# Optimization experiments

Hardware: AMD Instinct MI355X
Metric: run time of the kernel (lower is better)

## Reference

```python
import jax, jax.numpy as jnp
import numpy as np

B, D_IN, H, D_OUT = 8192, 1024, 4096, 1024


def setup_inputs() -> dict:
    key = jax.random.key(0)
    ks = jax.random.split(key, 8)
    return {
        "X": jax.random.normal(ks[0], (B, D_IN), jnp.float32),
        "state": jax.random.normal(ks[1], (B, H), jnp.float32),
        "W_in": jax.random.normal(ks[2], (H, D_IN), jnp.float32) * (2.0 / D_IN) ** 0.5,
        "b_in": jax.random.normal(ks[3], (H,), jnp.float32) * 0.1,
        "W_rec": jax.random.normal(ks[4], (H, H), jnp.float32) * (2.0 / H) ** 0.5,
        "b_rec": jax.random.normal(ks[5], (H,), jnp.float32) * 0.1,
        "W_out": jax.random.normal(ks[6], (D_OUT, H), jnp.float32) * (2.0 / H) ** 0.5,
        "b_out": jax.random.normal(ks[7], (D_OUT,), jnp.float32) * 0.1,
    }


def reference(X, state, W_in, b_in, W_rec, b_rec, W_out, b_out):
    # Single vanilla RNN cell step (ReLU recurrence), matching VanillaRNN.forward.
    # state: [B, H] = ReLU(X @ W_in^T + b_in + state @ W_rec^T + b_rec)
    new_state = jax.nn.relu(X @ W_in.T + b_in + state @ W_rec.T + b_rec)
    # out: [B, D_OUT] = ReLU(new_state @ W_out^T + b_out)
    out = jax.nn.relu(new_state @ W_out.T + b_out)
    return out, new_state
```

## Files before the change

### kernel.cpp

```cpp
#include <hip/hip_runtime.h>
#include <hip/hip_bf16.h>
#include <stdint.h>
#include <stddef.h>

#define BSZ  8192
#define DIN  1024
#define HH   4096
#define DOUT 1024

#define BM 128
#define BN 128
#define BK 32

typedef __attribute__((ext_vector_type(8))) short   frag8;
typedef __attribute__((ext_vector_type(4))) float   f32x4;
typedef __attribute__((ext_vector_type(8))) unsigned short u16x8;

__device__ __forceinline__ unsigned short f2bf_rne(float f) {
    union { float f; uint32_t u; } c; c.f = f;
    uint32_t u = c.u;
    return (unsigned short)((u + 0x7FFFu + ((u >> 16) & 1u)) >> 16);
}

__device__ __forceinline__ void cvt8(const float* __restrict__ s, unsigned short* __restrict__ d) {
    f32x4 v0 = *(const f32x4*)s;
    f32x4 v1 = *(const f32x4*)(s + 4);
    u16x8 o;
    o[0] = f2bf_rne(v0[0]); o[1] = f2bf_rne(v0[1]); o[2] = f2bf_rne(v0[2]); o[3] = f2bf_rne(v0[3]);
    o[4] = f2bf_rne(v1[0]); o[5] = f2bf_rne(v1[1]); o[6] = f2bf_rne(v1[2]); o[7] = f2bf_rne(v1[3]);
    *(u16x8*)d = o;
}

__global__ __launch_bounds__(256)
void cvt_f32_bf16(const float* __restrict__ src, unsigned short* __restrict__ dst, long n) {
    long i = ((long)blockIdx.x * 256 + threadIdx.x) * 8;
    if (i < n) cvt8(src + i, dst + i);
}

__global__ __launch_bounds__(256)
void cvt_all5(const float* __restrict__ s0, unsigned short* __restrict__ d0, long n0,
              const float* __restrict__ s1, unsigned short* __restrict__ d1, long n1,
              const float* __restrict__ s2, unsigned short* __restrict__ d2, long n2,
              const float* __restrict__ s3, unsigned short* __restrict__ d3, long n3,
              const float* __restrict__ s4, unsigned short* __restrict__ d4, long n4) {
    long i = ((long)blockIdx.x * 256 + threadIdx.x) * 8;
    if (i < n0) { cvt8(s0 + i, d0 + i); return; } i -= n0;
    if (i < n1) { cvt8(s1 + i, d1 + i); return; } i -= n1;
    if (i < n2) { cvt8(s2 + i, d2 + i); return; } i -= n2;
    if (i < n3) { cvt8(s3 + i, d3 + i); return; } i -= n3;
    if (i < n4) { cvt8(s4 + i, d4 + i); }
}

#define NX8  ((long)BSZ * DIN / 8)
#define NS8  ((long)BSZ * HH / 8)
#define NWI8 ((long)HH * DIN / 8)
#define NWR8 ((long)HH * HH / 8)
#define NWO8 ((long)DOUT * HH / 8)
#define NCVT_BLOCKS 32768

__global__ __launch_bounds__(256)
void cvt_pack(const float* __restrict__ X, const float* __restrict__ S,
              const float* __restrict__ Wi, const float* __restrict__ Wr,
              const float* __restrict__ Wo,
              unsigned short* __restrict__ XS, unsigned short* __restrict__ W1,
              unsigned short* __restrict__ Wob) {
    long i = (long)blockIdx.x * 256 + threadIdx.x;
    if (i < NX8)  { long r = i >> 7, c = i & 127; cvt8(X + i * 8, XS + r * 5120 + c * 8); return; }
    i -= NX8;
    if (i < NS8)  { long r = i >> 9, c = i & 511; cvt8(S + i * 8, XS + r * 5120 + 1024 + c * 8); return; }
    i -= NS8;
    if (i < NWI8) { long r = i >> 7, c = i & 127; cvt8(Wi + i * 8, W1 + r * 5120 + c * 8); return; }
    i -= NWI8;
    if (i < NWR8) { long r = i >> 9, c = i & 511; cvt8(Wr + i * 8, W1 + r * 5120 + 1024 + c * 8); return; }
    i -= NWR8;
    if (i < NWO8) { cvt8(Wo + i * 8, Wob + i * 8); }
}

__device__ __forceinline__ void glds16(const unsigned short* __restrict__ gp, short* lp) {
    __builtin_amdgcn_global_load_lds(
        (const __attribute__((address_space(1))) uint32_t*)gp,
        (__attribute__((address_space(3))) uint32_t*)lp, 16, 0, 0);
}

__device__ __forceinline__ void glds16v(const unsigned short* __restrict__ gp, void* lp) {
    __builtin_amdgcn_global_load_lds(
        (const __attribute__((address_space(1))) uint32_t*)gp,
        (__attribute__((address_space(3))) uint32_t*)lp, 16, 0, 0);
}

template<int C>
__device__ __forceinline__ void ktile_group(
    int kA, int kB,
    const unsigned short* __restrict__ gA, size_t a64,
    const unsigned short* __restrict__ gB, size_t b64,
    const char* Ar0, const char* Br0, char* ldsw,
    int aoff, int boff, f32x4 (&acc)[8][4])
{
    const char* Ar = Ar0 + C * 65536;
    const char* Br = Br0 + C * 65536;
    char* wA = ldsw + (C ^ 1) * 65536;
    char* wB = ldsw + C * 65536 + 32768;
    const unsigned short* gAk = gA + kA * 64;
    const unsigned short* gBk = gB + kB * 64;

    frag8 bfr[4][2];
    frag8 af[2][2];
#pragma unroll
    for (int p = 0; p < 4; ++p) {
        if (p == 0) {
#pragma unroll
            for (int ni = 0; ni < 4; ni++)
#pragma unroll
                for (int ks = 0; ks < 2; ks++)
                    bfr[ni][ks] = *(const frag8*)(Br + ni * 2048 + (boff ^ (ks << 6)));
        }
#pragma unroll
        for (int m2 = 0; m2 < 2; m2++)
#pragma unroll
            for (int ks = 0; ks < 2; ks++)
                af[m2][ks] = *(const frag8*)(Ar + (p * 2 + m2) * 2048 + (aoff ^ (ks << 6)));

        if (p == 0) {
            glds16v(gAk,           wA);
            glds16v(gAk + a64,     wA + 8192);
            glds16v(gAk + 2 * a64, wA + 16384);
            glds16v(gAk + 3 * a64, wA + 16384 + 8192);
        } else if (p == 1) {
            glds16v(gBk,           wB);
            glds16v(gBk + b64,     wB + 8192);
        } else if (p == 2) {
            glds16v(gBk + 2 * b64, wB + 16384);
            glds16v(gBk + 3 * b64, wB + 16384 + 8192);
        }

        __builtin_amdgcn_s_barrier();
        __builtin_amdgcn_s_setprio(1);
#pragma unroll
        for (int m2 = 0; m2 < 2; m2++)
#pragma unroll
            for (int ni = 0; ni < 4; ni++)
#pragma unroll
                for (int ks = 0; ks < 2; ks++)
                    acc[p * 2 + m2][ni] = __builtin_amdgcn_mfma_f32_16x16x32_bf16(
                        af[m2][ks], bfr[ni][ks], acc[p * 2 + m2][ni], 0, 0, 0);
        __builtin_amdgcn_s_setprio(0);
        if (p == 3) asm volatile("s_waitcnt vmcnt(4)" ::: "memory");
        __builtin_amdgcn_s_barrier();
    }
}

__global__ __launch_bounds__(512, 2)
void gemm256_relu(const unsigned short* __restrict__ A, int lda,
                  const unsigned short* __restrict__ B, int ldb, int K,
                  const float* __restrict__ bias1, const float* __restrict__ bias2,
                  float* __restrict__ C, unsigned short* __restrict__ Cb, int ncols) {
    extern __shared__ char lds[];

    const int tid  = threadIdx.x;
    const int wave = tid >> 6, lane = tid & 63;
    const int quad = lane >> 4, l16 = lane & 15;
    const int wm2  = wave >> 2, wn4 = wave & 3;
    const int tile_m = blockIdx.y * 256;
    const int tile_n = blockIdx.x * 256;
    const int NT = K >> 6;

    const int r0 = tid >> 3;
    const int c0 = (tid & 7) ^ (r0 & 7);
    const unsigned short* gA = A + (size_t)(tile_m + r0) * lda + c0 * 8;
    const unsigned short* gB = B + (size_t)(tile_n + r0) * ldb + c0 * 8;
    const size_t a64 = (size_t)64 * lda, b64 = (size_t)64 * ldb;

    const int swz  = (quad ^ (l16 & 7)) << 4;
    const int aoff = l16 * 128 + swz;
    const int boff = ((wn4 & 1) * 64 + l16) * 128 + swz;
    const char* Ar0 = lds + wm2 * 16384;
    const char* Br0 = lds + 32768 + (wn4 >> 1) * 16384;
    char* ldsw = lds + wave * 1024;

    glds16v(gA,           ldsw);
    glds16v(gA + a64,     ldsw + 8192);
    glds16v(gA + 2 * a64, ldsw + 16384);
    glds16v(gA + 3 * a64, ldsw + 16384 + 8192);
    glds16v(gB,           ldsw + 32768);
    glds16v(gB + b64,     ldsw + 32768 + 8192);
    glds16v(gB + 2 * b64, ldsw + 32768 + 16384);
    glds16v(gB + 3 * b64, ldsw + 32768 + 16384 + 8192);
    {
        const unsigned short* gB1 = gB + 64;
        glds16v(gB1,           ldsw + 65536 + 32768);
        glds16v(gB1 + b64,     ldsw + 65536 + 32768 + 8192);
        glds16v(gB1 + 2 * b64, ldsw + 65536 + 32768 + 16384);
        glds16v(gB1 + 3 * b64, ldsw + 65536 + 32768 + 16384 + 8192);
    }
    asm volatile("s_waitcnt vmcnt(4)" ::: "memory");
    __builtin_amdgcn_s_barrier();

    f32x4 acc[8][4] = {};

    for (int kt = 0; kt < NT; kt += 2) {
        int kA0 = kt + 1;
        int kB0 = kt + 2; if (kB0 >= NT) kB0 -= NT;
        ktile_group<0>(kA0, kB0, gA, a64, gB, b64, Ar0, Br0, ldsw, aoff, boff, acc);
        int kA1 = kt + 2; if (kA1 >= NT) kA1 -= NT;
        int kB1 = kt + 3; if (kB1 >= NT) kB1 -= NT;
        ktile_group<1>(kA1, kB1, gA, a64, gB, b64, Ar0, Br0, ldsw, aoff, boff, acc);
    }

#pragma unroll
    for (int ni = 0; ni < 4; ni++) {
        const int n = tile_n + wn4 * 64 + ni * 16 + l16;
        float bv = bias1[n];
        if (bias2) bv += bias2[n];
#pragma unroll
        for (int mi = 0; mi < 8; mi++) {
            const int m0 = tile_m + wm2 * 128 + mi * 16 + quad * 4;
#pragma unroll
            for (int r = 0; r < 4; r++) {
                float v = acc[mi][ni][r] + bv;
                v = v > 0.f ? v : 0.f;
                const size_t idx = (size_t)(m0 + r) * ncols + n;
                C[idx] = v;
                if (Cb) Cb[idx] = f2bf_rne(v);
            }
        }
    }
}

template <bool A_BF16, bool B_BF16>
__global__ __launch_bounds__(256)
void gemm_bt_relu(const void* __restrict__ A1, int lda1,
                  const void* __restrict__ A2, int lda2,
                  const void* __restrict__ B1, int ldb1,
                  const void* __restrict__ B2, int ldb2,
                  int Ksplit, int K,
                  const float* __restrict__ bias1, const float* __restrict__ bias2,
                  float* __restrict__ C, unsigned short* __restrict__ Cb, int N) {
    __shared__ short As[BM * BK];
    __shared__ short Bs[BN * BK];

    const int tid    = threadIdx.x;
    const int tile_m = blockIdx.y * BM;
    const int tile_n = blockIdx.x * BN;
    const int wave = tid >> 6, lane = tid & 63;
    const int quad = lane >> 4, l16 = lane & 15;
    const int wm = (wave >> 1) * 64;
    const int wn = (wave & 1) * 64;
    const int sr = tid >> 2;
    const int sc = (tid & 3) * 8;

    short* ldsA0 = &As[tid * 8]; short* ldsA1 = &As[(256 + tid) * 8];
    short* ldsB0 = &Bs[tid * 8]; short* ldsB1 = &Bs[(256 + tid) * 8];

    f32x4 acc[4][4] = {};

    for (int phase = 0; phase < 2; ++phase) {
        const int kmax = phase ? (K - Ksplit) : Ksplit;
        if (kmax <= 0) continue;
        const void* Ap = phase ? A2 : A1; const int la = phase ? lda2 : lda1;
        const void* Bp = phase ? B2 : B1; const int lb = phase ? ldb2 : ldb1;

        const unsigned short *ga = nullptr, *gb = nullptr;
        const float *fa = nullptr, *fb = nullptr;
        if (A_BF16) ga = (const unsigned short*)Ap + (size_t)(tile_m + sr) * la + sc;
        else        fa = (const float*)Ap          + (size_t)(tile_m + sr) * la + sc;
        if (B_BF16) gb = (const unsigned short*)Bp + (size_t)(tile_n + sr) * lb + sc;
        else        fb = (const float*)Bp          + (size_t)(tile_n + sr) * lb + sc;
        const size_t la64 = (size_t)64 * la, lb64 = (size_t)64 * lb;

        for (int kk = 0; kk < kmax; kk += BK) {
            __syncthreads();
            if (A_BF16) {
                glds16(ga, ldsA0); glds16(ga + la64, ldsA1); ga += BK;
            } else {
                unsigned short t0[8], t1[8];
                cvt8(fa, t0); cvt8(fa + la64, t1); fa += BK;
                *(u16x8*)ldsA0 = *(u16x8*)t0; *(u16x8*)ldsA1 = *(u16x8*)t1;
            }
            if (B_BF16) {
                glds16(gb, ldsB0); glds16(gb + lb64, ldsB1); gb += BK;
            } else {
                unsigned short t0[8], t1[8];
                cvt8(fb, t0); cvt8(fb + lb64, t1); fb += BK;
                *(u16x8*)ldsB0 = *(u16x8*)t0; *(u16x8*)ldsB1 = *(u16x8*)t1;
            }
            __syncthreads();

            frag8 af2[4], bfr[4];
#pragma unroll
            for (int i = 0; i < 4; i++)
                af2[i] = *(const frag8*)&As[(wm + i * 16 + l16) * BK + quad * 8];
#pragma unroll
            for (int i = 0; i < 4; i++)
                bfr[i] = *(const frag8*)&Bs[(wn + i * 16 + l16) * BK + quad * 8];
#pragma unroll
            for (int mi = 0; mi < 4; mi++)
#pragma unroll
                for (int ni = 0; ni < 4; ni++)
                    acc[mi][ni] = __builtin_amdgcn_mfma_f32_16x16x32_bf16(
                        af2[mi], bfr[ni], acc[mi][ni], 0, 0, 0);
        }
    }

#pragma unroll
    for (int mi = 0; mi < 4; mi++) {
        const int m0 = tile_m + wm + mi * 16 + quad * 4;
#pragma unroll
        for (int ni = 0; ni < 4; ni++) {
            const int n = tile_n + wn + ni * 16 + l16;
            float bv = bias1[n];
            if (bias2) bv += bias2[n];
#pragma unroll
            for (int r = 0; r < 4; r++) {
                float v = acc[mi][ni][r] + bv;
                v = v > 0.f ? v : 0.f;
                const size_t idx = (size_t)(m0 + r) * N + n;
                C[idx] = v;
                if (Cb) Cb[idx] = f2bf_rne(v);
            }
        }
    }
}

extern "C" void kernel_launch(void* const* d_in, const int* in_sizes, int n_in,
                              void* d_out, int out_size, void* d_ws, size_t ws_size,
                              hipStream_t stream) {
    const float* X     = (const float*)d_in[0];
    const float* state = (const float*)d_in[1];
    const float* W_in  = (const float*)d_in[2];
    const float* b_in  = (const float*)d_in[3];
    const float* W_rec = (const float*)d_in[4];
    const float* b_rec = (const float*)d_in[5];
    const float* W_out = (const float*)d_in[6];
    const float* b_out = (const float*)d_in[7];

    float* out       = (float*)d_out;
    float* new_state = out + (size_t)BSZ * DOUT;

    const size_t nX = (size_t)BSZ * DIN, nS = (size_t)BSZ * HH;
    const size_t nWin = (size_t)HH * DIN, nWrec = (size_t)HH * HH, nWout = (size_t)DOUT * HH;

    const size_t offXS = 0;
    const size_t offW1 = offXS + (size_t)BSZ * (DIN + HH) * 2;
    const size_t offWo = offW1 + (size_t)HH  * (DIN + HH) * 2;
    const size_t offNS = offWo + (size_t)DOUT * HH * 2;
    const size_t need_full = offNS + nS * 2;
    const size_t need_mid = nS * 2 + nWout * 2;

    char* ws = (char*)d_ws;
    const dim3 blk(256);

    if (ws_size >= need_full) {
        unsigned short* XSb = (unsigned short*)(ws + offXS);
        unsigned short* W1b = (unsigned short*)(ws + offW1);
        unsigned short* Wob = (unsigned short*)(ws + offWo);
        unsigned short* NSb = (unsigned short*)(ws + offNS);

        static bool s_attr = false;
        if (!s_attr) {
            hipFuncSetAttribute(reinterpret_cast<const void*>(gemm256_relu),
                                hipFuncAttributeMaxDynamicSharedMemorySize, 131072);
            s_attr = true;
        }

        cvt_pack<<<dim3(NCVT_BLOCKS), blk, 0, stream>>>(
            X, state, W_in, W_rec, W_out, XSb, W1b, Wob);
        gemm256_relu<<<dim3(HH / 256, BSZ / 256), dim3(512), 131072, stream>>>(
            XSb, DIN + HH, W1b, DIN + HH, DIN + HH, b_in, b_rec, new_state, NSb, HH);
        gemm256_relu<<<dim3(DOUT / 256, BSZ / 256), dim3(512), 131072, stream>>>(
            NSb, HH, Wob, HH, HH, b_out, nullptr, out, nullptr, DOUT);
    } else if (ws_size >= need_mid) {
        const dim3 g1(HH / BN, BSZ / BM);
        const dim3 g2(DOUT / BN, BSZ / BM);
        unsigned short* NSb   = (unsigned short*)ws;
        unsigned short* Woutb = (unsigned short*)(ws + nS * 2);
        cvt_f32_bf16<<<dim3((unsigned)((nWout / 8 + 255) / 256)), blk, 0, stream>>>(
            W_out, Woutb, (long)nWout);
        gemm_bt_relu<false, false><<<g1, blk, 0, stream>>>(
            X, DIN, state, HH, W_in, DIN, W_rec, HH, DIN, DIN + HH,
            b_in, b_rec, new_state, NSb, HH);
        gemm_bt_relu<true, true><<<g2, blk, 0, stream>>>(
            NSb, HH, NSb, HH, Woutb, HH, Woutb, HH, HH, HH,
            b_out, nullptr, out, nullptr, DOUT);
    } else {
        const dim3 g1(HH / BN, BSZ / BM);
        const dim3 g2(DOUT / BN, BSZ / BM);
        gemm_bt_relu<false, false><<<g1, blk, 0, stream>>>(
            X, DIN, state, HH, W_in, DIN, W_rec, HH, DIN, DIN + HH,
            b_in, b_rec, new_state, nullptr, HH);
        gemm_bt_relu<false, false><<<g2, blk, 0, stream>>>(
            new_state, HH, new_state, HH, W_out, HH, W_out, HH, HH, HH,
            b_out, nullptr, out, nullptr, DOUT);
    }
}
```

Baseline: 750.7 us.

## Register double-buffer fragments, cut barriers, and use 128-row tiles for output GEMM

Reworks the GEMM k-loop so LDS fragments for the next phase and next k-tile are prefetched into double-buffered registers. This drops from two barriers per phase to two per k-tile. The kernel is templated on the number of M rows per tile, and the second GEMM (N=1024) launches with 128-row tiles so it has twice as many blocks, which should fill the GPU better. The costs are higher register pressure from the duplicated fragment arrays and subtle correctness risk in the reworked barrier and waitcnt placement.

```diff
diff --git a/kernel.cpp b/kernel.cpp
--- a/kernel.cpp
+++ b/kernel.cpp
@@ -35,20 +35,6 @@
 void cvt_f32_bf16(const float* __restrict__ src, unsigned short* __restrict__ dst, long n) {
     long i = ((long)blockIdx.x * 256 + threadIdx.x) * 8;
     if (i < n) cvt8(src + i, dst + i);
-}
-
-__global__ __launch_bounds__(256)
-void cvt_all5(const float* __restrict__ s0, unsigned short* __restrict__ d0, long n0,
-              const float* __restrict__ s1, unsigned short* __restrict__ d1, long n1,
-              const float* __restrict__ s2, unsigned short* __restrict__ d2, long n2,
-              const float* __restrict__ s3, unsigned short* __restrict__ d3, long n3,
-              const float* __restrict__ s4, unsigned short* __restrict__ d4, long n4) {
-    long i = ((long)blockIdx.x * 256 + threadIdx.x) * 8;
-    if (i < n0) { cvt8(s0 + i, d0 + i); return; } i -= n0;
-    if (i < n1) { cvt8(s1 + i, d1 + i); return; } i -= n1;
-    if (i < n2) { cvt8(s2 + i, d2 + i); return; } i -= n2;
-    if (i < n3) { cvt8(s3 + i, d3 + i); return; } i -= n3;
-    if (i < n4) { cvt8(s4 + i, d4 + i); }
 }
 
 #define NX8  ((long)BSZ * DIN / 8)
@@ -88,52 +74,56 @@
         (__attribute__((address_space(3))) uint32_t*)lp, 16, 0, 0);
 }
 
-template<int C>
-__device__ __forceinline__ void ktile_group(
-    int kA, int kB,
+template<int MR, int C>
+__device__ __forceinline__ void ktile(
     const unsigned short* __restrict__ gA, size_t a64,
     const unsigned short* __restrict__ gB, size_t b64,
-    const char* Ar0, const char* Br0, char* ldsw,
-    int aoff, int boff, f32x4 (&acc)[8][4])
+    int kA, int kB,
+    const char* ArB, const char* BrB, char* wAB, char* wBB,
+    int aoff, int boff,
+    frag8 (&bfr)[2][4][2], frag8 (&af)[2][2][2], f32x4 (&acc)[MR][4])
 {
-    const char* Ar = Ar0 + C * 65536;
-    const char* Br = Br0 + C * 65536;
-    char* wA = ldsw + (C ^ 1) * 65536;
-    char* wB = ldsw + C * 65536 + 32768;
-    const unsigned short* gAk = gA + kA * 64;
-    const unsigned short* gBk = gB + kB * 64;
-
-    frag8 bfr[4][2];
-    frag8 af[2][2];
-#pragma unroll
-    for (int p = 0; p < 4; ++p) {
-        if (p == 0) {
+    constexpr int NPH    = MR / 2;
+    constexpr int ABYTES = MR * 4096;
+    constexpr int BUFSTR = ABYTES + 32768;
+    const char* Ar  = ArB + C * BUFSTR;
+    const char* ArN = ArB + (C ^ 1) * BUFSTR;
+    const char* BrN = BrB + (C ^ 1) * BUFSTR;
+    char* wA = wAB + (C ^ 1) * BUFSTR;
+    char* wB = wBB + C * BUFSTR;
+    const unsigned short* gAk = gA + (size_t)kA * 64;
+    const unsigned short* gBk = gB + (size_t)kB * 64;
+
+#pragma unroll
+    for (int i = 0; i < NPH; ++i)
+        glds16v(gAk + (size_t)i * a64, wA + i * 8192);
+#pragma unroll
+    for (int i = 0; i < 4; ++i)
+        glds16v(gBk + (size_t)i * b64, wB + i * 8192);
+
+#pragma unroll
+    for (int p = 0; p < NPH; ++p) {
+        if (p < NPH - 1) {
+#pragma unroll
+            for (int m2 = 0; m2 < 2; m2++)
+#pragma unroll
+                for (int ks = 0; ks < 2; ks++)
+                    af[(p + 1) & 1][m2][ks] =
+                        *(const frag8*)(Ar + ((p + 1) * 2 + m2) * 2048 + (aoff ^ (ks << 6)));
+        } else {
 #pragma unroll
             for (int ni = 0; ni < 4; ni++)
 #pragma unroll
                 for (int ks = 0; ks < 2; ks++)
-                    bfr[ni][ks] = *(const frag8*)(Br + ni * 2048 + (boff ^ (ks << 6)));
-        }
-#pragma unroll
-        for (int m2 = 0; m2 < 2; m2++)
-#pragma unroll
-            for (int ks = 0; ks < 2; ks++)
-                af[m2][ks] = *(const frag8*)(Ar + (p * 2 + m2) * 2048 + (aoff ^ (ks << 6)));
-
-        if (p == 0) {
-            glds16v(gAk,           wA);
-            glds16v(gAk + a64,     wA + 8192);
-            glds16v(gAk + 2 * a64, wA + 16384);
-            glds16v(gAk + 3 * a64, wA + 16384 + 8192);
-        } else if (p == 1) {
-            glds16v(gBk,           wB);
-            glds16v(gBk + b64,     wB + 8192);
-        } else if (p == 2) {
-            glds16v(gBk + 2 * b64, wB + 16384);
-            glds16v(gBk + 3 * b64, wB + 16384 + 8192);
-        }
-
-        __builtin_amdgcn_s_barrier();
+                    bfr[C ^ 1][ni][ks] =
+                        *(const frag8*)(BrN + ni * 2048 + (boff ^ (ks << 6)));
+#pragma unroll
+            for (int m2 = 0; m2 < 2; m2++)
+#pragma unroll
+                for (int ks = 0; ks < 2; ks++)
+                    af[0][m2][ks] =
+                        *(const frag8*)(ArN + m2 * 2048 + (aoff ^ (ks << 6)));
+        }
         __builtin_amdgcn_s_setprio(1);
 #pragma unroll
         for (int m2 = 0; m2 < 2; m2++)
@@ -142,25 +132,36 @@
 #pragma unroll
                 for (int ks = 0; ks < 2; ks++)
                     acc[p * 2 + m2][ni] = __builtin_amdgcn_mfma_f32_16x16x32_bf16(
-                        af[m2][ks], bfr[ni][ks], acc[p * 2 + m2][ni], 0, 0, 0);
+                        af[p & 1][m2][ks], bfr[C][ni][ks], acc[p * 2 + m2][ni], 0, 0, 0);
         __builtin_amdgcn_s_setprio(0);
-        if (p == 3) asm volatile("s_waitcnt vmcnt(4)" ::: "memory");
-        __builtin_amdgcn_s_barrier();
-    }
-}
-
+        if (p == NPH - 2) {
+            asm volatile("s_waitcnt vmcnt(4)" ::: "memory");
+            __builtin_amdgcn_sched_barrier(0);
+            __builtin_amdgcn_s_barrier();
+            __builtin_amdgcn_sched_barrier(0);
+        }
+    }
+    asm volatile("s_waitcnt lgkmcnt(0)" ::: "memory");
+    __builtin_amdgcn_sched_barrier(0);
+    __builtin_amdgcn_s_barrier();
+    __builtin_amdgcn_sched_barrier(0);
+}
+
+template<int MR>
 __global__ __launch_bounds__(512, 2)
 void gemm256_relu(const unsigned short* __restrict__ A, int lda,
                   const unsigned short* __restrict__ B, int ldb, int K,
                   const float* __restrict__ bias1, const float* __restrict__ bias2,
                   float* __restrict__ C, unsigned short* __restrict__ Cb, int ncols) {
     extern __shared__ char lds[];
+    constexpr int ABYTES = MR * 4096;
+    constexpr int BUFSTR = ABYTES + 32768;
 
     const int tid  = threadIdx.x;
     const int wave = tid >> 6, lane = tid & 63;
     const int quad = lane >> 4, l16 = lane & 15;
     const int wm2  = wave >> 2, wn4 = wave & 3;
-    const int tile_m = blockIdx.y * 256;
+    const int tile_m = blockIdx.y * (MR * 32);
     const int tile_n = blockIdx.x * 256;
     const int NT = K >> 6;
 
@@ -173,37 +174,47 @@
     const int swz  = (quad ^ (l16 & 7)) << 4;
     const int aoff = l16 * 128 + swz;
     const int boff = ((wn4 & 1) * 64 + l16) * 128 + swz;
-    const char* Ar0 = lds + wm2 * 16384;
-    const char* Br0 = lds + 32768 + (wn4 >> 1) * 16384;
-    char* ldsw = lds + wave * 1024;
-
-    glds16v(gA,           ldsw);
-    glds16v(gA + a64,     ldsw + 8192);
-    glds16v(gA + 2 * a64, ldsw + 16384);
-    glds16v(gA + 3 * a64, ldsw + 16384 + 8192);
-    glds16v(gB,           ldsw + 32768);
-    glds16v(gB + b64,     ldsw + 32768 + 8192);
-    glds16v(gB + 2 * b64, ldsw + 32768 + 16384);
-    glds16v(gB + 3 * b64, ldsw + 32768 + 16384 + 8192);
-    {
-        const unsigned short* gB1 = gB + 64;
-        glds16v(gB1,           ldsw + 65536 + 32768);
-        glds16v(gB1 + b64,     ldsw + 65536 + 32768 + 8192);
-        glds16v(gB1 + 2 * b64, ldsw + 65536 + 32768 + 16384);
-        glds16v(gB1 + 3 * b64, ldsw + 65536 + 32768 + 16384 + 8192);
-    }
+    const char* ArB = lds + wm2 * (MR * 2048);
+    const char* BrB = lds + ABYTES + (wn4 >> 1) * 16384;
+    char* wAB = lds + wave * 1024;
+    char* wBB = lds + ABYTES + wave * 1024;
+
+    frag8 bfr[2][4][2];
+    frag8 af[2][2][2];
+    f32x4 acc[MR][4] = {};
+
+#pragma unroll
+    for (int i = 0; i < MR / 2; ++i) glds16v(gA + (size_t)i * a64, wAB + i * 8192);
+#pragma unroll
+    for (int i = 0; i < 4; ++i)      glds16v(gB + (size_t)i * b64, wBB + i * 8192);
+#pragma unroll
+    for (int i = 0; i < 4; ++i)      glds16v(gB + 64 + (size_t)i * b64, wBB + BUFSTR + i * 8192);
     asm volatile("s_waitcnt vmcnt(4)" ::: "memory");
+    __builtin_amdgcn_sched_barrier(0);
     __builtin_amdgcn_s_barrier();
-
-    f32x4 acc[8][4] = {};
+    __builtin_amdgcn_sched_barrier(0);
+#pragma unroll
+    for (int ni = 0; ni < 4; ni++)
+#pragma unroll
+        for (int ks = 0; ks < 2; ks++)
+            bfr[0][ni][ks] = *(const frag8*)(BrB + ni * 2048 + (boff ^ (ks << 6)));
+#pragma unroll
+    for (int m2 = 0; m2 < 2; m2++)
+#pragma unroll
+        for (int ks = 0; ks < 2; ks++)
+            af[0][m2][ks] = *(const frag8*)(ArB + m2 * 2048 + (aoff ^ (ks << 6)));
+    asm volatile("s_waitcnt lgkmcnt(0)" ::: "memory");
+    __builtin_amdgcn_sched_barrier(0);
+    __builtin_amdgcn_s_barrier();
+    __builtin_amdgcn_sched_barrier(0);
 
     for (int kt = 0; kt < NT; kt += 2) {
-        int kA0 = kt + 1;
-        int kB0 = kt + 2; if (kB0 >= NT) kB0 -= NT;
-        ktile_group<0>(kA0, kB0, gA, a64, gB, b64, Ar0, Br0, ldsw, aoff, boff, acc);
-        int kA1 = kt + 2; if (kA1 >= NT) kA1 -= NT;
-        int kB1 = kt + 3; if (kB1 >= NT) kB1 -= NT;
-        ktile_group<1>(kA1, kB1, gA, a64, gB, b64, Ar0, Br0, ldsw, aoff, boff, acc);
+        const int kA0 = kt + 1;
+        const int kB0 = (kt + 2 < NT) ? kt + 2 : 0;
+        ktile<MR, 0>(gA, a64, gB, b64, kA0, kB0, ArB, BrB, wAB, wBB, aoff, boff, bfr, af, acc);
+        const int kA1 = (kt + 2 < NT) ? kt + 2 : 0;
+        const int kB1 = (kt + 3 < NT) ? kt + 3 : 1;
+        ktile<MR, 1>(gA, a64, gB, b64, kA1, kB1, ArB, BrB, wAB, wBB, aoff, boff, bfr, af, acc);
     }
 
 #pragma unroll
@@ -212,8 +223,8 @@
         float bv = bias1[n];
         if (bias2) bv += bias2[n];
 #pragma unroll
-        for (int mi = 0; mi < 8; mi++) {
-            const int m0 = tile_m + wm2 * 128 + mi * 16 + quad * 4;
+        for (int mi = 0; mi < MR; mi++) {
+            const int m0 = tile_m + wm2 * (MR * 16) + mi * 16 + quad * 4;
 #pragma unroll
             for (int r = 0; r < 4; r++) {
                 float v = acc[mi][ni][r] + bv;
@@ -336,8 +347,8 @@
     float* out       = (float*)d_out;
     float* new_state = out + (size_t)BSZ * DOUT;
 
-    const size_t nX = (size_t)BSZ * DIN, nS = (size_t)BSZ * HH;
-    const size_t nWin = (size_t)HH * DIN, nWrec = (size_t)HH * HH, nWout = (size_t)DOUT * HH;
+    const size_t nS = (size_t)BSZ * HH;
+    const size_t nWout = (size_t)DOUT * HH;
 
     const size_t offXS = 0;
     const size_t offW1 = offXS + (size_t)BSZ * (DIN + HH) * 2;
@@ -357,16 +368,18 @@
 
         static bool s_attr = false;
         if (!s_attr) {
-            hipFuncSetAttribute(reinterpret_cast<const void*>(gemm256_relu),
+            hipFuncSetAttribute(reinterpret_cast<const void*>(gemm256_relu<8>),
                                 hipFuncAttributeMaxDynamicSharedMemorySize, 131072);
+            hipFuncSetAttribute(reinterpret_cast<const void*>(gemm256_relu<4>),
+                                hipFuncAttributeMaxDynamicSharedMemorySize, 98304);
             s_attr = true;
         }
 
         cvt_pack<<<dim3(NCVT_BLOCKS), blk, 0, stream>>>(
             X, state, W_in, W_rec, W_out, XSb, W1b, Wob);
-        gemm256_relu<<<dim3(HH / 256, BSZ / 256), dim3(512), 131072, stream>>>(
+        gemm256_relu<8><<<dim3(HH / 256, BSZ / 256), dim3(512), 131072, stream>>>(
             XSb, DIN + HH, W1b, DIN + HH, DIN + HH, b_in, b_rec, new_state, NSb, HH);
-        gemm256_relu<<<dim3(DOUT / 256, BSZ / 256), dim3(512), 131072, stream>>>(
+        gemm256_relu<4><<<dim3(DOUT / 256, BSZ / 128), dim3(512), 98304, stream>>>(
             NSb, HH, Wob, HH, HH, b_out, nullptr, out, nullptr, DOUT);
     } else if (ws_size >= need_mid) {
         const dim3 g1(HH / BN, BSZ / BM);
```

After: 897.6 us. +19.6%, slower.
